# Performance work log

Hardware: AMD Instinct MI355X
Metric: run time of the kernel (lower is better)

Reference implementation:

```python
import jax, jax.numpy as jnp
import numpy as np

B, N, Y, C = 8, 512, 64, 256


def setup_inputs() -> dict:
    key = jax.random.key(0)
    ks = jax.random.split(key, 7)
    sampled = jax.random.normal(ks[0], (B, N, Y, C), dtype=jnp.float32)
    # binary visibility mask (original passes 0/1-ish validity)
    valid = jnp.round(jax.random.uniform(ks[1], (B, N, Y), dtype=jnp.float32))
    # buffer: normalized y depth steps, y_steps = arange(Y)
    y_steps = jnp.arange(Y, dtype=jnp.float32)
    y_norm = (y_steps - y_steps.min()) / jnp.maximum(y_steps.max() - y_steps.min(), 1e-6)
    # weight_mlp = Linear(C+1 -> C), GELU, Linear(C -> 1); store weights pre-transposed (in, out)
    s1 = 1.0 / np.sqrt(C + 1)
    s2 = 1.0 / np.sqrt(C)
    W1 = jax.random.uniform(ks[2], (C + 1, C), dtype=jnp.float32, minval=-s1, maxval=s1)
    b1 = jax.random.uniform(ks[3], (C,), dtype=jnp.float32, minval=-s1, maxval=s1)
    W2 = jax.random.uniform(ks[4], (C, 1), dtype=jnp.float32, minval=-s2, maxval=s2)
    b2 = jax.random.uniform(ks[5], (1,), dtype=jnp.float32, minval=-s2, maxval=s2)
    return {"sampled": sampled, "valid": valid, "y_norm": y_norm,
            "W1": W1, "b1": b1, "W2": W2, "b2": b2}


def reference(sampled, valid, y_norm, W1, b1, W2, b2):
    b, n, y, c = sampled.shape
    yfeat = jnp.broadcast_to(y_norm.reshape(1, 1, y, 1), (b, n, y, 1))
    feat = jnp.concatenate([sampled, yfeat], axis=-1)            # [B,N,Y,C+1]
    h = jax.nn.gelu(feat @ W1 + b1, approximate=False)            # [B,N,Y,C]
    logits = (h @ W2 + b2)[..., 0]                                # [B,N,Y]
    logits = jnp.where(valid < 0.5, jnp.float32(-10000.0), logits)
    weights = jax.nn.softmax(logits, axis=-1) * valid
    denom = jnp.maximum(weights.sum(axis=-1, keepdims=True), 1e-6)
    weights = weights / denom
    return jnp.einsum('bnyc,bny->bnc', sampled, weights)          # [B,N,C]
```

## Files before the change

kernel.cpp:

```cpp
#include <hip/hip_runtime.h>

#define NTOK 4096
#define AST  264

using short8  = __attribute__((ext_vector_type(8))) short;
using floatx4 = __attribute__((ext_vector_type(4))) float;

static __device__ __forceinline__ float bf2f(short s) {
  union { unsigned u; float f; } v; v.u = ((unsigned)(unsigned short)s) << 16;
  return v.f;
}

static __device__ __forceinline__ unsigned cvt_pk_bf16(float lo, float hi) {
  unsigned d;
  asm("v_cvt_pk_bf16_f32 %0, %1, %2" : "=v"(d) : "v"(lo), "v"(hi));
  return d;
}

static __device__ __forceinline__ float fast_gelu(float z) {
  float x  = z * 0.70710678118654752f;
  float ax = fabsf(x);
  float t  = __builtin_amdgcn_rcpf(fmaf(0.47047f, ax, 1.0f));
  float em = __expf(-ax * ax);
  float p  = fmaf(fmaf(0.7478556f, t, -0.0958798f), t, 0.3480242f);
  float er = fmaf(-(p * t), em, 1.0f);
  unsigned sgn = __float_as_uint(x) & 0x80000000u;
  er = __uint_as_float(__float_as_uint(er) | sgn);
  return z * fmaf(0.5f, er, 0.5f);
}

__global__ void prep_w1(const float* __restrict__ W1, short* __restrict__ W1s) {
  const int n  = threadIdx.x;
  const int kb = blockIdx.x;
  const int s  = kb >> 2;
  const int l  = ((kb & 3) << 4) | (n & 15);
  const int t  = n >> 4;
  float f[8];
  #pragma unroll
  for (int j = 0; j < 8; ++j) f[j] = W1[(kb * 8 + j) * 256 + n];
  uint4 u;
  u.x = cvt_pk_bf16(f[0], f[1]);
  u.y = cvt_pk_bf16(f[2], f[3]);
  u.z = cvt_pk_bf16(f[4], f[5]);
  u.w = cvt_pk_bf16(f[6], f[7]);
  *(uint4*)(W1s + (((s * 16 + t) * 64 + l) << 3)) = u;
}

__global__ void __launch_bounds__(512, 4) agg_kernel(
    const float* __restrict__ sampled, const float* __restrict__ valid,
    const float* __restrict__ y_norm, const float* __restrict__ W1,
    const float* __restrict__ b1, const float* __restrict__ W2,
    const float* __restrict__ b2, const short* __restrict__ W1s,
    float* __restrict__ out) {
  __shared__ __align__(16) short Abf[64 * AST];
  __shared__ float wlog[8][64];
  __shared__ float ynl[64];
  __shared__ float ph[256];

  const int tid = threadIdx.x;
  const int tok = blockIdx.x;
  const int wv  = tid >> 6;
  const int ln  = tid & 63;
  const int q   = ln >> 4;
  const int c15 = ln & 15;
  const float* S = sampled + ((size_t)tok << 14);

  if (tid < 64) ynl[tid] = y_norm[tid];

  const float4* S4 = (const float4*)S;
  float4 v[8];
  #pragma unroll
  for (int it = 0; it < 8; ++it) v[it] = S4[it * 512 + tid];

  short8 bfr[16];
  #pragma unroll
  for (int s = 0; s < 8; ++s)
    #pragma unroll
    for (int nt = 0; nt < 2; ++nt)
      bfr[s * 2 + nt] =
          *(const short8*)(W1s + (((s * 16 + wv * 2 + nt) * 64 + ln) << 3));

  #pragma unroll
  for (int it = 0; it < 8; ++it) {
    int j  = it * 512 + tid;
    int y  = j >> 6;
    int k4 = (j & 63) << 2;
    uint2 dd;
    dd.x = cvt_pk_bf16(v[it].x, v[it].y);
    dd.y = cvt_pk_bf16(v[it].z, v[it].w);
    *(uint2*)(&Abf[y * AST + k4]) = dd;
  }
  __syncthreads();

  const floatx4 fzero = {0.f, 0.f, 0.f, 0.f};
  floatx4 acc[4][2];
  #pragma unroll
  for (int mt = 0; mt < 4; ++mt)
    #pragma unroll
    for (int nt = 0; nt < 2; ++nt) acc[mt][nt] = fzero;

  #pragma unroll
  for (int s = 0; s < 8; ++s) {
    short8 af[4];
    #pragma unroll
    for (int mt = 0; mt < 4; ++mt)
      af[mt] = *(const short8*)(&Abf[(mt * 16 + c15) * AST + s * 32 + q * 8]);
    #pragma unroll
    for (int nt = 0; nt < 2; ++nt)
      #pragma unroll
      for (int mt = 0; mt < 4; ++mt)
        acc[mt][nt] = __builtin_amdgcn_mfma_f32_16x16x32_bf16(
            af[mt], bfr[s * 2 + nt], acc[mt][nt], 0, 0, 0);
  }

  float w2v[2], b1v[2], wlv[2];
  #pragma unroll
  for (int nt = 0; nt < 2; ++nt) {
    int n = wv * 32 + nt * 16 + c15;
    w2v[nt] = W2[n];
    b1v[nt] = b1[n];
    wlv[nt] = W1[65536 + n];
  }
  #pragma unroll
  for (int mt = 0; mt < 4; ++mt) {
    #pragma unroll
    for (int r = 0; r < 4; ++r) {
      int m = mt * 16 + q * 4 + r;
      float ym = ynl[m];
      float p = 0.f;
      #pragma unroll
      for (int nt = 0; nt < 2; ++nt) {
        float z = acc[mt][nt][r] + ym * wlv[nt] + b1v[nt];
        p += fast_gelu(z) * w2v[nt];
      }
      p += __shfl_xor(p, 1);
      p += __shfl_xor(p, 2);
      p += __shfl_xor(p, 4);
      p += __shfl_xor(p, 8);
      if (c15 == 0) wlog[wv][m] = p;
    }
  }
  __syncthreads();

  float lg = ((wlog[0][ln] + wlog[1][ln]) + (wlog[2][ln] + wlog[3][ln]))
           + ((wlog[4][ln] + wlog[5][ln]) + (wlog[6][ln] + wlog[7][ln])) + b2[0];
  float vv = valid[tok * 64 + ln];
  float lm = (vv < 0.5f) ? -10000.0f : lg;
  float mx = lm;
  #pragma unroll
  for (int d = 32; d > 0; d >>= 1) mx = fmaxf(mx, __shfl_xor(mx, d));
  float e  = __expf(lm - mx);
  float s1 = e;
  #pragma unroll
  for (int d = 32; d > 0; d >>= 1) s1 += __shfl_xor(s1, d);
  float wgt = e / s1 * vv;
  float s2  = wgt;
  #pragma unroll
  for (int d = 32; d > 0; d >>= 1) s2 += __shfl_xor(s2, d);
  wgt = wgt / fmaxf(s2, 1e-6f);

  float a0 = 0.f;
  if (tid < 256) {
    #pragma unroll
    for (int y = 0; y < 32; ++y) {
      float wy = __shfl(wgt, y);
      a0 = fmaf(bf2f(Abf[y * AST + tid]), wy, a0);
    }
  } else {
    const int c = tid - 256;
    #pragma unroll
    for (int y = 32; y < 64; ++y) {
      float wy = __shfl(wgt, y);
      a0 = fmaf(bf2f(Abf[y * AST + c]), wy, a0);
    }
    ph[c] = a0;
  }
  __syncthreads();
  if (tid < 256) out[(size_t)tok * 256 + tid] = a0 + ph[tid];
}

extern "C" void kernel_launch(void* const* d_in, const int* in_sizes, int n_in,
                              void* d_out, int out_size, void* d_ws, size_t ws_size,
                              hipStream_t stream) {
  const float* sampled = (const float*)d_in[0];
  const float* valid   = (const float*)d_in[1];
  const float* y_norm  = (const float*)d_in[2];
  const float* W1      = (const float*)d_in[3];
  const float* b1      = (const float*)d_in[4];
  const float* W2      = (const float*)d_in[5];
  const float* b2      = (const float*)d_in[6];
  short* W1s = (short*)d_ws;
  float* out = (float*)d_out;

  prep_w1<<<32, 256, 0, stream>>>(W1, W1s);
  agg_kernel<<<NTOK, 512, 0, stream>>>(sampled, valid, y_norm, W1, b1, W2, b2, W1s, out);
}
```

Before: 400.5 us.

## Process 16 tokens per block with register prefetch of the next token

```diff
diff --git a/kernel.cpp b/kernel.cpp
--- a/kernel.cpp
+++ b/kernel.cpp
@@ -1,6 +1,8 @@
 #include <hip/hip_runtime.h>
 
 #define NTOK 4096
+#define TPB  16
+#define NBLK (NTOK / TPB)
 #define AST  264
 
 using short8  = __attribute__((ext_vector_type(8))) short;
@@ -46,31 +48,33 @@
   *(uint4*)(W1s + (((s * 16 + t) * 64 + l) << 3)) = u;
 }
 
-__global__ void __launch_bounds__(512, 4) agg_kernel(
+__global__ void __launch_bounds__(512, 2) agg_kernel(
     const float* __restrict__ sampled, const float* __restrict__ valid,
     const float* __restrict__ y_norm, const float* __restrict__ W1,
     const float* __restrict__ b1, const float* __restrict__ W2,
     const float* __restrict__ b2, const short* __restrict__ W1s,
     float* __restrict__ out) {
   __shared__ __align__(16) short Abf[64 * AST];
-  __shared__ float wlog[8][64];
+  __shared__ float wlog[8 * 64];
   __shared__ float ynl[64];
   __shared__ float ph[256];
 
-  const int tid = threadIdx.x;
-  const int tok = blockIdx.x;
-  const int wv  = tid >> 6;
-  const int ln  = tid & 63;
-  const int q   = ln >> 4;
-  const int c15 = ln & 15;
-  const float* S = sampled + ((size_t)tok << 14);
+  const int tid  = threadIdx.x;
+  const int wv   = tid >> 6;
+  const int ln   = tid & 63;
+  const int q    = ln >> 4;
+  const int c15  = ln & 15;
+  const int tok0 = blockIdx.x * TPB;
 
   if (tid < 64) ynl[tid] = y_norm[tid];
 
-  const float4* S4 = (const float4*)S;
   float4 v[8];
-  #pragma unroll
-  for (int it = 0; it < 8; ++it) v[it] = S4[it * 512 + tid];
+  {
+    const float4* S4 = (const float4*)(sampled + ((size_t)tok0 << 14));
+    #pragma unroll
+    for (int it = 0; it < 8; ++it) v[it] = S4[it * 512 + tid];
+  }
+  float vnext = valid[tok0 * 64 + ln];
 
   short8 bfr[16];
   #pragma unroll
@@ -79,39 +83,6 @@
     for (int nt = 0; nt < 2; ++nt)
       bfr[s * 2 + nt] =
           *(const short8*)(W1s + (((s * 16 + wv * 2 + nt) * 64 + ln) << 3));
-
-  #pragma unroll
-  for (int it = 0; it < 8; ++it) {
-    int j  = it * 512 + tid;
-    int y  = j >> 6;
-    int k4 = (j & 63) << 2;
-    uint2 dd;
-    dd.x = cvt_pk_bf16(v[it].x, v[it].y);
-    dd.y = cvt_pk_bf16(v[it].z, v[it].w);
-    *(uint2*)(&Abf[y * AST + k4]) = dd;
-  }
-  __syncthreads();
-
-  const floatx4 fzero = {0.f, 0.f, 0.f, 0.f};
-  floatx4 acc[4][2];
-  #pragma unroll
-  for (int mt = 0; mt < 4; ++mt)
-    #pragma unroll
-    for (int nt = 0; nt < 2; ++nt) acc[mt][nt] = fzero;
-
-  #pragma unroll
-  for (int s = 0; s < 8; ++s) {
-    short8 af[4];
-    #pragma unroll
-    for (int mt = 0; mt < 4; ++mt)
-      af[mt] = *(const short8*)(&Abf[(mt * 16 + c15) * AST + s * 32 + q * 8]);
-    #pragma unroll
-    for (int nt = 0; nt < 2; ++nt)
-      #pragma unroll
-      for (int mt = 0; mt < 4; ++mt)
-        acc[mt][nt] = __builtin_amdgcn_mfma_f32_16x16x32_bf16(
-            af[mt], bfr[s * 2 + nt], acc[mt][nt], 0, 0, 0);
-  }
 
   float w2v[2], b1v[2], wlv[2];
   #pragma unroll
@@ -121,62 +92,124 @@
     b1v[nt] = b1[n];
     wlv[nt] = W1[65536 + n];
   }
-  #pragma unroll
-  for (int mt = 0; mt < 4; ++mt) {
-    #pragma unroll
-    for (int r = 0; r < 4; ++r) {
-      int m = mt * 16 + q * 4 + r;
-      float ym = ynl[m];
-      float p = 0.f;
-      #pragma unroll
-      for (int nt = 0; nt < 2; ++nt) {
-        float z = acc[mt][nt][r] + ym * wlv[nt] + b1v[nt];
-        p += fast_gelu(z) * w2v[nt];
-      }
-      p += __shfl_xor(p, 1);
-      p += __shfl_xor(p, 2);
-      p += __shfl_xor(p, 4);
-      p += __shfl_xor(p, 8);
-      if (c15 == 0) wlog[wv][m] = p;
+  const float b2v = b2[0];
+
+  float a0 = 0.f;
+
+  for (int t = 0; t < TPB; ++t) {
+    __syncthreads();
+    if (t > 0 && tid < 256)
+      out[(size_t)(tok0 + t - 1) * 256 + tid] = a0 + ph[tid];
+
+    {
+      short* wp = Abf + wv * AST + (ln << 2);
+      #pragma unroll
+      for (int it = 0; it < 8; ++it) {
+        uint2 dd;
+        dd.x = cvt_pk_bf16(v[it].x, v[it].y);
+        dd.y = cvt_pk_bf16(v[it].z, v[it].w);
+        *(uint2*)(wp + it * 8 * AST) = dd;
+      }
+    }
+    float vv = vnext;
+    __syncthreads();
+
+    if (t + 1 < TPB) {
+      const float4* Sn = (const float4*)(sampled + ((size_t)(tok0 + t + 1) << 14));
+      #pragma unroll
+      for (int it = 0; it < 8; ++it) v[it] = Sn[it * 512 + tid];
+      vnext = valid[(tok0 + t + 1) * 64 + ln];
+    }
+
+    const floatx4 fzero = {0.f, 0.f, 0.f, 0.f};
+    floatx4 acc[4][2];
+    #pragma unroll
+    for (int mt = 0; mt < 4; ++mt)
+      #pragma unroll
+      for (int nt = 0; nt < 2; ++nt) acc[mt][nt] = fzero;
+
+    const short* ap = Abf + c15 * AST + q * 8;
+    #pragma unroll
+    for (int s = 0; s < 8; ++s) {
+      short8 af[4];
+      #pragma unroll
+      for (int mt = 0; mt < 4; ++mt)
+        af[mt] = *(const short8*)(ap + mt * 16 * AST + s * 32);
+      #pragma unroll
+      for (int nt = 0; nt < 2; ++nt)
+        #pragma unroll
+        for (int mt = 0; mt < 4; ++mt)
+          acc[mt][nt] = __builtin_amdgcn_mfma_f32_16x16x32_bf16(
+              af[mt], bfr[s * 2 + nt], acc[mt][nt], 0, 0, 0);
+    }
+
+    #pragma unroll
+    for (int mt = 0; mt < 4; ++mt) {
+      #pragma unroll
+      for (int r = 0; r < 4; ++r) {
+        int m = mt * 16 + q * 4 + r;
+        float ym = ynl[m];
+        float p = 0.f;
+        #pragma unroll
+        for (int nt = 0; nt < 2; ++nt) {
+          float z = acc[mt][nt][r] + ym * wlv[nt] + b1v[nt];
+          p += fast_gelu(z) * w2v[nt];
+        }
+        p += __shfl_xor(p, 1);
+        p += __shfl_xor(p, 2);
+        p += __shfl_xor(p, 4);
+        p += __shfl_xor(p, 8);
+        if (c15 == 0) wlog[wv * 64 + m] = p;
+      }
+    }
+    __syncthreads();
+
+    float lg = ((wlog[0 * 64 + ln] + wlog[1 * 64 + ln]) +
+                (wlog[2 * 64 + ln] + wlog[3 * 64 + ln])) +
+               ((wlog[4 * 64 + ln] + wlog[5 * 64 + ln]) +
+                (wlog[6 * 64 + ln] + wlog[7 * 64 + ln])) + b2v;
+    float lm = (vv < 0.5f) ? -10000.0f : lg;
+    float mx = lm;
+    #pragma unroll
+    for (int d = 32; d > 0; d >>= 1) mx = fmaxf(mx, __shfl_xor(mx, d));
+    float e  = __expf(lm - mx);
+    float s1 = e;
+    #pragma unroll
+    for (int d = 32; d > 0; d >>= 1) s1 += __shfl_xor(s1, d);
+    float wgt = e / s1 * vv;
+    float s2  = wgt;
+    #pragma unroll
+    for (int d = 32; d > 0; d >>= 1) s2 += __shfl_xor(s2, d);
+    wgt = wgt / fmaxf(s2, 1e-6f);
+
+    if (tid < 256) {
+      const short* Ac = Abf + tid;
+      float p0 = 0.f, p1 = 0.f, p2 = 0.f, p3 = 0.f;
+      #pragma unroll
+      for (int y = 0; y < 32; y += 4) {
+        p0 = fmaf(bf2f(Ac[(y + 0) * AST]), __shfl(wgt, y + 0), p0);
+        p1 = fmaf(bf2f(Ac[(y + 1) * AST]), __shfl(wgt, y + 1), p1);
+        p2 = fmaf(bf2f(Ac[(y + 2) * AST]), __shfl(wgt, y + 2), p2);
+        p3 = fmaf(bf2f(Ac[(y + 3) * AST]), __shfl(wgt, y + 3), p3);
+      }
+      a0 = (p0 + p1) + (p2 + p3);
+    } else {
+      const short* Ac = Abf + (tid - 256);
+      float p0 = 0.f, p1 = 0.f, p2 = 0.f, p3 = 0.f;
+      #pragma unroll
+      for (int y = 32; y < 64; y += 4) {
+        p0 = fmaf(bf2f(Ac[(y + 0) * AST]), __shfl(wgt, y + 0), p0);
+        p1 = fmaf(bf2f(Ac[(y + 1) * AST]), __shfl(wgt, y + 1), p1);
+        p2 = fmaf(bf2f(Ac[(y + 2) * AST]), __shfl(wgt, y + 2), p2);
+        p3 = fmaf(bf2f(Ac[(y + 3) * AST]), __shfl(wgt, y + 3), p3);
+      }
+      ph[tid - 256] = (p0 + p1) + (p2 + p3);
     }
   }
+
   __syncthreads();
-
-  float lg = ((wlog[0][ln] + wlog[1][ln]) + (wlog[2][ln] + wlog[3][ln]))
-           + ((wlog[4][ln] + wlog[5][ln]) + (wlog[6][ln] + wlog[7][ln])) + b2[0];
-  float vv = valid[tok * 64 + ln];
-  float lm = (vv < 0.5f) ? -10000.0f : lg;
-  float mx = lm;
-  #pragma unroll
-  for (int d = 32; d > 0; d >>= 1) mx = fmaxf(mx, __shfl_xor(mx, d));
-  float e  = __expf(lm - mx);
-  float s1 = e;
-  #pragma unroll
-  for (int d = 32; d > 0; d >>= 1) s1 += __shfl_xor(s1, d);
-  float wgt = e / s1 * vv;
-  float s2  = wgt;
-  #pragma unroll
-  for (int d = 32; d > 0; d >>= 1) s2 += __shfl_xor(s2, d);
-  wgt = wgt / fmaxf(s2, 1e-6f);
-
-  float a0 = 0.f;
-  if (tid < 256) {
-    #pragma unroll
-    for (int y = 0; y < 32; ++y) {
-      float wy = __shfl(wgt, y);
-      a0 = fmaf(bf2f(Abf[y * AST + tid]), wy, a0);
-    }
-  } else {
-    const int c = tid - 256;
-    #pragma unroll
-    for (int y = 32; y < 64; ++y) {
-      float wy = __shfl(wgt, y);
-      a0 = fmaf(bf2f(Abf[y * AST + c]), wy, a0);
-    }
-    ph[c] = a0;
-  }
-  __syncthreads();
-  if (tid < 256) out[(size_t)tok * 256 + tid] = a0 + ph[tid];
+  if (tid < 256)
+    out[(size_t)(tok0 + TPB - 1) * 256 + tid] = a0 + ph[tid];
 }
 
 extern "C" void kernel_launch(void* const* d_in, const int* in_sizes, int n_in,
@@ -193,5 +226,5 @@
   float* out = (float*)d_out;
 
   prep_w1<<<32, 256, 0, stream>>>(W1, W1s);
-  agg_kernel<<<NTOK, 512, 0, stream>>>(sampled, valid, y_norm, W1, b1, W2, b2, W1s, out);
-}
+  agg_kernel<<<NBLK, 512, 0, stream>>>(sampled, valid, y_norm, W1, b1, W2, b2, W1s, out);
+}
```

New measurement: 403.0 us. About the same (+0.6%).

## Process sixteen tokens per block with register double-buffered prefetch

Applied to the files above, without the earlier changes.

```diff
diff --git a/kernel.cpp b/kernel.cpp
--- a/kernel.cpp
+++ b/kernel.cpp
@@ -1,15 +1,12 @@
 #include <hip/hip_runtime.h>
 
 #define NTOK 4096
+#define TPB  16
+#define NBLK (NTOK / TPB)
 #define AST  264
 
 using short8  = __attribute__((ext_vector_type(8))) short;
 using floatx4 = __attribute__((ext_vector_type(4))) float;
-
-static __device__ __forceinline__ float bf2f(short s) {
-  union { unsigned u; float f; } v; v.u = ((unsigned)(unsigned short)s) << 16;
-  return v.f;
-}
 
 static __device__ __forceinline__ unsigned cvt_pk_bf16(float lo, float hi) {
   unsigned d;
@@ -46,31 +43,34 @@
   *(uint4*)(W1s + (((s * 16 + t) * 64 + l) << 3)) = u;
 }
 
-__global__ void __launch_bounds__(512, 4) agg_kernel(
+__global__ void __launch_bounds__(512, 2) agg_kernel(
     const float* __restrict__ sampled, const float* __restrict__ valid,
     const float* __restrict__ y_norm, const float* __restrict__ W1,
     const float* __restrict__ b1, const float* __restrict__ W2,
     const float* __restrict__ b2, const short* __restrict__ W1s,
     float* __restrict__ out) {
   __shared__ __align__(16) short Abf[64 * AST];
-  __shared__ float wlog[8][64];
+  __shared__ float wlog[8 * 64];
   __shared__ float ynl[64];
-  __shared__ float ph[256];
-
-  const int tid = threadIdx.x;
-  const int tok = blockIdx.x;
-  const int wv  = tid >> 6;
-  const int ln  = tid & 63;
-  const int q   = ln >> 4;
-  const int c15 = ln & 15;
-  const float* S = sampled + ((size_t)tok << 14);
+  __shared__ float pw[8 * 256];
+
+  const int tid  = threadIdx.x;
+  const int wv   = tid >> 6;
+  const int ln   = tid & 63;
+  const int q    = ln >> 4;
+  const int c15  = ln & 15;
+  const int swv  = __builtin_amdgcn_readfirstlane(wv);
+  const int tok0 = blockIdx.x * TPB;
 
   if (tid < 64) ynl[tid] = y_norm[tid];
 
-  const float4* S4 = (const float4*)S;
-  float4 v[8];
-  #pragma unroll
-  for (int it = 0; it < 8; ++it) v[it] = S4[it * 512 + tid];
+  float4 vA[8], vB[8];
+  {
+    const float4* S4 = (const float4*)(sampled + ((size_t)tok0 << 14));
+    #pragma unroll
+    for (int it = 0; it < 8; ++it) vA[it] = S4[it * 512 + tid];
+  }
+  float vvA = valid[tok0 * 64 + ln], vvB = 0.f;
 
   short8 bfr[16];
   #pragma unroll
@@ -80,39 +80,6 @@
       bfr[s * 2 + nt] =
           *(const short8*)(W1s + (((s * 16 + wv * 2 + nt) * 64 + ln) << 3));
 
-  #pragma unroll
-  for (int it = 0; it < 8; ++it) {
-    int j  = it * 512 + tid;
-    int y  = j >> 6;
-    int k4 = (j & 63) << 2;
-    uint2 dd;
-    dd.x = cvt_pk_bf16(v[it].x, v[it].y);
-    dd.y = cvt_pk_bf16(v[it].z, v[it].w);
-    *(uint2*)(&Abf[y * AST + k4]) = dd;
-  }
-  __syncthreads();
-
-  const floatx4 fzero = {0.f, 0.f, 0.f, 0.f};
-  floatx4 acc[4][2];
-  #pragma unroll
-  for (int mt = 0; mt < 4; ++mt)
-    #pragma unroll
-    for (int nt = 0; nt < 2; ++nt) acc[mt][nt] = fzero;
-
-  #pragma unroll
-  for (int s = 0; s < 8; ++s) {
-    short8 af[4];
-    #pragma unroll
-    for (int mt = 0; mt < 4; ++mt)
-      af[mt] = *(const short8*)(&Abf[(mt * 16 + c15) * AST + s * 32 + q * 8]);
-    #pragma unroll
-    for (int nt = 0; nt < 2; ++nt)
-      #pragma unroll
-      for (int mt = 0; mt < 4; ++mt)
-        acc[mt][nt] = __builtin_amdgcn_mfma_f32_16x16x32_bf16(
-            af[mt], bfr[s * 2 + nt], acc[mt][nt], 0, 0, 0);
-  }
-
   float w2v[2], b1v[2], wlv[2];
   #pragma unroll
   for (int nt = 0; nt < 2; ++nt) {
@@ -121,62 +88,120 @@
     b1v[nt] = b1[n];
     wlv[nt] = W1[65536 + n];
   }
-  #pragma unroll
-  for (int mt = 0; mt < 4; ++mt) {
-    #pragma unroll
-    for (int r = 0; r < 4; ++r) {
-      int m = mt * 16 + q * 4 + r;
-      float ym = ynl[m];
-      float p = 0.f;
-      #pragma unroll
-      for (int nt = 0; nt < 2; ++nt) {
-        float z = acc[mt][nt][r] + ym * wlv[nt] + b1v[nt];
-        p += fast_gelu(z) * w2v[nt];
-      }
-      p += __shfl_xor(p, 1);
-      p += __shfl_xor(p, 2);
-      p += __shfl_xor(p, 4);
-      p += __shfl_xor(p, 8);
-      if (c15 == 0) wlog[wv][m] = p;
-    }
-  }
+
+#define TOKEN_ITER(VC, VN, VVC, VVN, T)                                        \
+  {                                                                            \
+     \
+    {                                                                          \
+      short* wp = Abf + wv * AST + (ln << 2);                                  \
+      _Pragma("unroll")                                                        \
+      for (int it = 0; it < 8; ++it) {                                         \
+        uint2 dd;                                                              \
+        dd.x = cvt_pk_bf16(VC[it].x, VC[it].y);                                \
+        dd.y = cvt_pk_bf16(VC[it].z, VC[it].w);                                \
+        *(uint2*)(wp + it * 8 * AST) = dd;                                     \
+      }                                                                        \
+    }                                                                          \
+    __syncthreads();                            \
+                     \
+    if ((T) + 1 < TPB) {                                                       \
+      const float4* Sn =                                                       \
+          (const float4*)(sampled + ((size_t)(tok0 + (T) + 1) << 14));         \
+      _Pragma("unroll")                                                        \
+      for (int it = 0; it < 8; ++it) VN[it] = Sn[it * 512 + tid];              \
+      VVN = valid[(tok0 + (T) + 1) * 64 + ln];                                 \
+    }                                                                          \
+                              \
+    if ((T) > 0 && tid < 256) {                                                \
+      float o = ((pw[0 * 256 + tid] + pw[1 * 256 + tid]) +                     \
+                 (pw[2 * 256 + tid] + pw[3 * 256 + tid])) +                    \
+                ((pw[4 * 256 + tid] + pw[5 * 256 + tid]) +                     \
+                 (pw[6 * 256 + tid] + pw[7 * 256 + tid]));                     \
+      out[(size_t)(tok0 + (T) - 1) * 256 + tid] = o;                           \
+    }                                                                          \
+              \
+    const floatx4 fzero = {0.f, 0.f, 0.f, 0.f};                                \
+    floatx4 acc[4][2];                                                         \
+    _Pragma("unroll")                                                          \
+    for (int mt = 0; mt < 4; ++mt) {                                           \
+      acc[mt][0] = fzero;                                                      \
+      acc[mt][1] = fzero;                                                      \
+    }                                                                          \
+    const short* ap = Abf + c15 * AST + q * 8;                                 \
+    _Pragma("unroll")                                                          \
+    for (int s = 0; s < 8; ++s) {                                              \
+      short8 af[4];                                                            \
+      _Pragma("unroll")                                                        \
+      for (int mt = 0; mt < 4; ++mt)                                           \
+        af[mt] = *(const short8*)(ap + mt * 16 * AST + s * 32);                \
+      _Pragma("unroll")                                                        \
+      for (int nt = 0; nt < 2; ++nt)                                           \
+        _Pragma("unroll")                                                      \
+        for (int mt = 0; mt < 4; ++mt)                                         \
+          acc[mt][nt] = __builtin_amdgcn_mfma_f32_16x16x32_bf16(               \
+              af[mt], bfr[s * 2 + nt], acc[mt][nt], 0, 0, 0);                  \
+    }                                                                          \
+             \
+    _Pragma("unroll")                                                          \
+    for (int mt = 0; mt < 4; ++mt) {                                           \
+      _Pragma("unroll")                                                        \
+      for (int r = 0; r < 4; ++r) {                                            \
+        int m = mt * 16 + q * 4 + r;                                           \
+        float ym = ynl[m];                                                     \
+        float z0 = acc[mt][0][r] + ym * wlv[0] + b1v[0];                       \
+        float z1 = acc[mt][1][r] + ym * wlv[1] + b1v[1];                       \
+        float p = fast_gelu(z0) * w2v[0] + fast_gelu(z1) * w2v[1];             \
+        p += __shfl_xor(p, 1);                                                 \
+        p += __shfl_xor(p, 2);                                                 \
+        p += __shfl_xor(p, 4);                                                 \
+        p += __shfl_xor(p, 8);                                                 \
+        if (c15 == 0) wlog[wv * 64 + m] = p;                                   \
+      }                                                                        \
+    }                                                                          \
+    __syncthreads();                \
+       \
+    float lg = ((wlog[0 * 64 + ln] + wlog[1 * 64 + ln]) +                      \
+                (wlog[2 * 64 + ln] + wlog[3 * 64 + ln])) +                     \
+               ((wlog[4 * 64 + ln] + wlog[5 * 64 + ln]) +                      \
+                (wlog[6 * 64 + ln] + wlog[7 * 64 + ln]));                      \
+    float lm = ((VVC) < 0.5f) ? -10000.0f : lg;                                \
+    float mx = lm;                                                             \
+    _Pragma("unroll")                                                          \
+    for (int d = 32; d > 0; d >>= 1) mx = fmaxf(mx, __shfl_xor(mx, d));        \
+    float e = __expf(lm - mx) * (VVC);                                         \
+    float sd = e;                                                              \
+    _Pragma("unroll")                                                          \
+    for (int d = 32; d > 0; d >>= 1) sd += __shfl_xor(sd, d);                  \
+    float wgt = e * __builtin_amdgcn_rcpf(fmaxf(sd, 1e-6f));                   \
+                  \
+         \
+    float4 part = {0.f, 0.f, 0.f, 0.f};                                        \
+    _Pragma("unroll")                                                          \
+    for (int it = 0; it < 8; ++it) {                                           \
+      float wy = __uint_as_float(__builtin_amdgcn_readlane(                    \
+          (int)__float_as_uint(wgt), it * 8 + swv));                           \
+      part.x = fmaf(VC[it].x, wy, part.x);                                     \
+      part.y = fmaf(VC[it].y, wy, part.y);                                     \
+      part.z = fmaf(VC[it].z, wy, part.z);                                     \
+      part.w = fmaf(VC[it].w, wy, part.w);                                     \
+    }                                                                          \
+    *(float4*)(pw + wv * 256 + (ln << 2)) = part;                              \
+  }
+
+  for (int tt = 0; tt < TPB; tt += 2) {
+    TOKEN_ITER(vA, vB, vvA, vvB, tt)
+    TOKEN_ITER(vB, vA, vvB, vvA, tt + 1)
+  }
+#undef TOKEN_ITER
+
   __syncthreads();
-
-  float lg = ((wlog[0][ln] + wlog[1][ln]) + (wlog[2][ln] + wlog[3][ln]))
-           + ((wlog[4][ln] + wlog[5][ln]) + (wlog[6][ln] + wlog[7][ln])) + b2[0];
-  float vv = valid[tok * 64 + ln];
-  float lm = (vv < 0.5f) ? -10000.0f : lg;
-  float mx = lm;
-  #pragma unroll
-  for (int d = 32; d > 0; d >>= 1) mx = fmaxf(mx, __shfl_xor(mx, d));
-  float e  = __expf(lm - mx);
-  float s1 = e;
-  #pragma unroll
-  for (int d = 32; d > 0; d >>= 1) s1 += __shfl_xor(s1, d);
-  float wgt = e / s1 * vv;
-  float s2  = wgt;
-  #pragma unroll
-  for (int d = 32; d > 0; d >>= 1) s2 += __shfl_xor(s2, d);
-  wgt = wgt / fmaxf(s2, 1e-6f);
-
-  float a0 = 0.f;
   if (tid < 256) {
-    #pragma unroll
-    for (int y = 0; y < 32; ++y) {
-      float wy = __shfl(wgt, y);
-      a0 = fmaf(bf2f(Abf[y * AST + tid]), wy, a0);
-    }
-  } else {
-    const int c = tid - 256;
-    #pragma unroll
-    for (int y = 32; y < 64; ++y) {
-      float wy = __shfl(wgt, y);
-      a0 = fmaf(bf2f(Abf[y * AST + c]), wy, a0);
-    }
-    ph[c] = a0;
-  }
-  __syncthreads();
-  if (tid < 256) out[(size_t)tok * 256 + tid] = a0 + ph[tid];
+    float o = ((pw[0 * 256 + tid] + pw[1 * 256 + tid]) +
+               (pw[2 * 256 + tid] + pw[3 * 256 + tid])) +
+              ((pw[4 * 256 + tid] + pw[5 * 256 + tid]) +
+               (pw[6 * 256 + tid] + pw[7 * 256 + tid]));
+    out[(size_t)(tok0 + TPB - 1) * 256 + tid] = o;
+  }
 }
 
 extern "C" void kernel_launch(void* const* d_in, const int* in_sizes, int n_in,
@@ -193,5 +218,5 @@
   float* out = (float*)d_out;
 
   prep_w1<<<32, 256, 0, stream>>>(W1, W1s);
-  agg_kernel<<<NTOK, 512, 0, stream>>>(sampled, valid, y_norm, W1, b1, W2, b2, W1s, out);
-}
+  agg_kernel<<<NBLK, 512, 0, stream>>>(sampled, valid, y_norm, W1, b1, W2, b2, W1s, out);
+}
```

After: 387.3 us. -3.3%, faster.
